# Kernel optimization log

Measured on AMD Instinct MI355X. Metric: run time of the kernel, lower is better.

## Reference

```python
import jax, jax.numpy as jnp
import numpy as np

N = 50000   # nodes
E = 409600  # edges
H = 2       # heads
C = 64      # per-head channels


def _seg_softmax(alpha, dst, n):
    # PyG-style softmax over edges grouped by destination node. alpha: [E, H]
    m = jax.ops.segment_max(alpha, dst, num_segments=n)
    m = jnp.where(jnp.isfinite(m), m, 0.0)
    ex = jnp.exp(alpha - m[dst])
    s = jax.ops.segment_sum(ex, dst, num_segments=n)
    return ex / (s[dst] + 1e-16)


def _tconv(x, src, dst, e, Wq, bq, Wk, bk, Wv, bv, We, Ws, bs, n):
    # PyG TransformerConv (concat=True, beta=False, root_weight=True, dropout=0)
    q = (x @ Wq + bq).reshape(n, H, C)
    k = (x @ Wk + bk).reshape(n, H, C)
    v = (x @ Wv + bv).reshape(n, H, C)
    eh = (e @ We).reshape(-1, H, C)          # lin_edge has no bias in PyG
    kj = k[src] + eh                          # [E, H, C]
    alpha = (q[dst] * kj).sum(-1) / jnp.sqrt(jnp.float32(C))  # [E, H]
    alpha = _seg_softmax(alpha, dst, n)
    msg = (v[src] + eh) * alpha[:, :, None]   # [E, H, C]
    out = jax.ops.segment_sum(msg, dst, num_segments=n).reshape(n, H * C)
    return out + x @ Ws + bs                  # root/skip connection


def setup_inputs() -> dict:
    key = jax.random.key(0)
    ks = jax.random.split(key, 32)

    def lin_w(k, i, o):
        return (jax.random.normal(k, (i, o), dtype=jnp.float32) / np.sqrt(i)).astype(jnp.float32)

    inp = {
        "x": jax.random.normal(ks[0], (N, 6), dtype=jnp.float32),
        "edge_index": jax.random.randint(ks[1], (2, E), 0, N, dtype=jnp.int32).astype(jnp.int64),
        "edge_attr": jax.random.normal(ks[2], (E, 1), dtype=jnp.float32),
        # edge encoder: Linear(1, 64)
        "We_enc": lin_w(ks[3], 1, 64), "be_enc": jnp.zeros((64,), jnp.float32),
        # conv1: TransformerConv(6, 64, heads=2, edge_dim=64)
        "Wq1": lin_w(ks[4], 6, H * C), "bq1": jnp.zeros((H * C,), jnp.float32),
        "Wk1": lin_w(ks[5], 6, H * C), "bk1": jnp.zeros((H * C,), jnp.float32),
        "Wv1": lin_w(ks[6], 6, H * C), "bv1": jnp.zeros((H * C,), jnp.float32),
        "We1": lin_w(ks[7], 64, H * C),
        "Ws1": lin_w(ks[8], 6, H * C), "bs1": jnp.zeros((H * C,), jnp.float32),
        # conv2: TransformerConv(128, 64, heads=2, edge_dim=64)
        "Wq2": lin_w(ks[9], 128, H * C), "bq2": jnp.zeros((H * C,), jnp.float32),
        "Wk2": lin_w(ks[10], 128, H * C), "bk2": jnp.zeros((H * C,), jnp.float32),
        "Wv2": lin_w(ks[11], 128, H * C), "bv2": jnp.zeros((H * C,), jnp.float32),
        "We2": lin_w(ks[12], 64, H * C),
        "Ws2": lin_w(ks[13], 128, H * C), "bs2": jnp.zeros((H * C,), jnp.float32),
        # fc: Linear(128, 1)
        "Wfc": lin_w(ks[14], 128, 1), "bfc": jnp.zeros((1,), jnp.float32),
    }
    return inp


def reference(x, edge_index, edge_attr,
              We_enc, be_enc,
              Wq1, bq1, Wk1, bk1, Wv1, bv1, We1, Ws1, bs1,
              Wq2, bq2, Wk2, bk2, Wv2, bv2, We2, Ws2, bs2,
              Wfc, bfc):
    src, dst = edge_index[0], edge_index[1]
    e = edge_attr @ We_enc + be_enc           # [E, 64]
    h = jax.nn.relu(_tconv(x, src, dst, e, Wq1, bq1, Wk1, bk1, Wv1, bv1, We1, Ws1, bs1, N))
    h = jax.nn.relu(_tconv(h, src, dst, e, Wq2, bq2, Wk2, bk2, Wv2, bv2, We2, Ws2, bs2, N))
    return h @ Wfc + bfc                      # [N, 1]
```

## Files before the change

kernel.cpp:

```cpp
#include <hip/hip_runtime.h>


#define HC 128

typedef __attribute__((ext_vector_type(8))) short bf16x8;
typedef __attribute__((ext_vector_type(4))) float f32x4;
#if __has_builtin(__builtin_amdgcn_fdot2_f32_bf16)
typedef __attribute__((ext_vector_type(2))) __bf16 bf16x2;
#define HAS_DOT2 1
#else
#define HAS_DOT2 0
#endif

__device__ __forceinline__ unsigned bf16_rne(float f) {
    unsigned u = __float_as_uint(f);
    return (u + 0x7fffu + ((u >> 16) & 1u)) >> 16;
}
__device__ __forceinline__ float blo(unsigned u) { return __uint_as_float(u << 16); }
__device__ __forceinline__ float bhi(unsigned u) { return __uint_as_float(u & 0xffff0000u); }

__global__ void k_uc(const float* __restrict__ We_enc, const float* __restrict__ be_enc,
                     const float* __restrict__ We1, const float* __restrict__ We2,
                     float* __restrict__ uc) {
    int c = threadIdx.x;
    float u1 = 0.f, c1 = 0.f, u2 = 0.f, c2 = 0.f;
    for (int j = 0; j < 64; ++j) {
        float we = We_enc[j], be = be_enc[j];
        float w1 = We1[j * HC + c], w2 = We2[j * HC + c];
        u1 += we * w1; c1 += be * w1;
        u2 += we * w2; c2 += be * w2;
    }
    uc[c] = u1; uc[HC + c] = c1; uc[2 * HC + c] = u2; uc[3 * HC + c] = c2;
}

__global__ __launch_bounds__(256) void k_wpack(
    const float* __restrict__ Wq, const float* __restrict__ Wk,
    const float* __restrict__ Wv, const float* __restrict__ Ws,
    unsigned short* __restrict__ Bph) {
    int t = blockIdx.x * 256 + threadIdx.x;
    int nn = t >> 7;
    int kk = t & 127;
    int mat = nn >> 7, c = nn & 127;
    const float* W = (mat == 0) ? Wq : (mat == 1) ? Wk : (mat == 2) ? Wv : Ws;
    Bph[nn * 128 + kk] = (unsigned short)bf16_rne(W[kk * 128 + c]);
}

__global__ __launch_bounds__(256) void k_hist(const int* __restrict__ ei, int* __restrict__ deg, int E) {
    int t = blockIdx.x * blockDim.x + threadIdx.x;
    if (t < E) atomicAdd(&deg[ei[E + t]], 1);
}

__global__ __launch_bounds__(256) void k_scan1(const int* __restrict__ deg, int* __restrict__ bsum, int n) {
    int t = blockIdx.x * 256 + threadIdx.x;
    int v = (t < n) ? deg[t] : 0;
#pragma unroll
    for (int off = 1; off < 64; off <<= 1) v += __shfl_xor(v, off);
    __shared__ int wsum[4];
    int lane = threadIdx.x & 63, w = threadIdx.x >> 6;
    if (lane == 0) wsum[w] = v;
    __syncthreads();
    if (threadIdx.x == 0) bsum[blockIdx.x] = wsum[0] + wsum[1] + wsum[2] + wsum[3];
}

__global__ __launch_bounds__(256) void k_scan2(int* __restrict__ bsum, int nb) {
    __shared__ int sh[256];
    int t = threadIdx.x;
    int v = (t < nb) ? bsum[t] : 0;
    sh[t] = v;
    __syncthreads();
    for (int off = 1; off < 256; off <<= 1) {
        int x = (t >= off) ? sh[t - off] : 0;
        __syncthreads();
        sh[t] += x;
        __syncthreads();
    }
    if (t < nb) bsum[t] = sh[t] - v;
}

__global__ __launch_bounds__(256) void k_scan3(int* __restrict__ deg, const int* __restrict__ bsum,
                                               int* __restrict__ rowptr, int n, int E) {
    int t = blockIdx.x * 256 + threadIdx.x;
    int tid = threadIdx.x;
    int v = (t < n) ? deg[t] : 0;
    __shared__ int sh[256];
    sh[tid] = v;
    __syncthreads();
    for (int off = 1; off < 256; off <<= 1) {
        int x = (tid >= off) ? sh[tid - off] : 0;
        __syncthreads();
        sh[tid] += x;
        __syncthreads();
    }
    if (t < n) { rowptr[t] = bsum[blockIdx.x] + sh[tid] - v; deg[t] = 0; }
    if (t == 0) rowptr[n] = E;
}

__global__ __launch_bounds__(256) void k_scatter(
    const int* __restrict__ ei, const float* __restrict__ ea,
    const int* __restrict__ rowptr, int* __restrict__ cursor,
    int* __restrict__ srcs, float* __restrict__ eas, int E) {
    int t = blockIdx.x * blockDim.x + threadIdx.x;
    if (t >= E) return;
    int dst = ei[E + t];
    int pos = rowptr[dst] + atomicAdd(&cursor[dst], 1);
    srcs[pos] = ei[t];
    eas[pos] = ea[t];
}

__global__ __launch_bounds__(256) void k_lin6(
    const float* __restrict__ X, int n,
    const float* __restrict__ Wq, const float* __restrict__ bq,
    const float* __restrict__ Wk, const float* __restrict__ bk,
    const float* __restrict__ Wv, const float* __restrict__ bv,
    const float* __restrict__ Ws, const float* __restrict__ bs,
    unsigned short* __restrict__ q16, unsigned short* __restrict__ kv,
    unsigned short* __restrict__ sk) {
    __shared__ float xs[16][6];
    const int base = blockIdx.x * 16;
    const int tid = threadIdx.x;
    for (int i = tid; i < 16 * 6; i += 256) {
        int ni = base + i / 6;
        xs[i / 6][i % 6] = (ni < n) ? X[(size_t)ni * 6 + (i % 6)] : 0.f;
    }
    __syncthreads();
    const int c = tid & 127;
    const int m = tid >> 7;
    const float* WA = m ? Wv : Wq;
    const float* WB = m ? Ws : Wk;
    float accA[16], accB[16];
#pragma unroll
    for (int i = 0; i < 16; ++i) { accA[i] = 0.f; accB[i] = 0.f; }
    for (int j = 0; j < 6; ++j) {
        float w0 = WA[j * HC + c];
        float w1 = WB[j * HC + c];
#pragma unroll
        for (int i = 0; i < 16; ++i) {
            float xv = xs[i][j];
            accA[i] += xv * w0;
            accB[i] += xv * w1;
        }
    }
    if (m == 0) {
        const float bA = bq[c], bB = bk[c];
#pragma unroll
        for (int i = 0; i < 16; ++i) {
            int ni = base + i;
            if (ni < n) {
                q16[(size_t)ni * HC + c] = (unsigned short)bf16_rne(accA[i] + bA);
                kv[(size_t)ni * 256 + c] = (unsigned short)bf16_rne(accB[i] + bB);
            }
        }
    } else {
        const float bA = bv[c], bB = bs[c];
#pragma unroll
        for (int i = 0; i < 16; ++i) {
            int ni = base + i;
            if (ni < n) {
                kv[(size_t)ni * 256 + 128 + c] = (unsigned short)bf16_rne(accA[i] + bA);
                sk[(size_t)ni * HC + c] = (unsigned short)bf16_rne(accB[i] + bB);
            }
        }
    }
}

__global__ __launch_bounds__(256, 4) void k_lin2(
    const unsigned short* __restrict__ hb, const unsigned short* __restrict__ Bph,
    const float* __restrict__ bq, const float* __restrict__ bk,
    const float* __restrict__ bv, const float* __restrict__ bs,
    unsigned short* __restrict__ q16, unsigned short* __restrict__ kv,
    unsigned short* __restrict__ sk, int n) {
    __shared__ unsigned short Bs[128][128];
    const int tid = threadIdx.x;
    const int wid = tid >> 6, l = tid & 63;
    const int la = l & 15, lk = l >> 4;
    const int mb = blockIdx.x * 64;
    int nodeA = mb + wid * 16 + la;
    if (nodeA >= n) nodeA = n - 1;
    const int sw = (la & 7) << 3;
    const int crow0 = mb + wid * 16 + lk * 4;

    bf16x8 areg[4];
#pragma unroll
    for (int ks = 0; ks < 4; ++ks)
        areg[ks] = *(const bf16x8*)&hb[(size_t)nodeA * 128 + lk * 8 + ks * 32];

    for (int cq = 0; cq < 4; ++cq) {
        if (cq) __syncthreads();
        for (int i = tid; i < 128 * 16; i += 256) {
            int kk8 = i & 15;
            int nnl = i >> 4;
            bf16x8 val = *(const bf16x8*)&Bph[((size_t)(cq * 128 + nnl)) * 128 + kk8 * 8];
            int swk = (kk8 ^ (nnl & 7)) * 8;
            *(bf16x8*)&Bs[nnl][swk] = val;
        }
        __syncthreads();

        f32x4 acc[8];
#pragma unroll
        for (int nt = 0; nt < 8; ++nt) acc[nt] = (f32x4){0.f, 0.f, 0.f, 0.f};
#pragma unroll
        for (int ks = 0; ks < 4; ++ks) {
            const int rk = (lk * 8 + ks * 32) ^ sw;
#pragma unroll
            for (int nt = 0; nt < 8; ++nt) {
                bf16x8 Bh = *(const bf16x8*)&Bs[nt * 16 + la][rk];
                acc[nt] = __builtin_amdgcn_mfma_f32_16x16x32_bf16(areg[ks], Bh, acc[nt], 0, 0, 0);
            }
        }
        const float* bias = (cq == 0) ? bq : (cq == 1) ? bk : (cq == 2) ? bv : bs;
#pragma unroll
        for (int nt = 0; nt < 8; ++nt) {
            const int col = nt * 16 + la;
            const float bb = bias[col];
            if (cq == 0 || cq == 3) {
                unsigned short* out = (cq == 0) ? q16 : sk;
#pragma unroll
                for (int j = 0; j < 4; ++j) {
                    int n0 = crow0 + j;
                    if (n0 < n) out[(size_t)n0 * 128 + col] = (unsigned short)bf16_rne(acc[nt][j] + bb);
                }
            } else {
                const int co = (cq == 1) ? col : 128 + col;
#pragma unroll
                for (int j = 0; j < 4; ++j) {
                    int n0 = crow0 + j;
                    if (n0 < n) kv[(size_t)n0 * 256 + co] = (unsigned short)bf16_rne(acc[nt][j] + bb);
                }
            }
        }
    }
}

template <int MODE>
__global__ __launch_bounds__(256) void k_attn(
    const unsigned short* __restrict__ q16, const unsigned short* __restrict__ kvp,
    const int* __restrict__ rowptr, const int* __restrict__ srcs, const float* __restrict__ eas,
    const float* __restrict__ ucu, const float* __restrict__ ucc,
    const unsigned short* __restrict__ io, unsigned short* __restrict__ hb,
    const float* __restrict__ Wfc, const float* __restrict__ bfc,
    float* __restrict__ out, int n) {
    int wid = (int)((blockIdx.x * (size_t)blockDim.x + threadIdx.x) >> 6);
    int lane = threadIdx.x & 63;
    if (wid >= n) return;
    const int grp = lane >> 4;
    const int hl = lane & 15;
    const int ch = hl * 8;

    uint4 qp = *(const uint4*)&q16[(size_t)wid * 128 + ch];
    float qu, qc;
    {
        float qf0 = blo(qp.x), qf1 = bhi(qp.x), qf2 = blo(qp.y), qf3 = bhi(qp.y);
        float qf4 = blo(qp.z), qf5 = bhi(qp.z), qf6 = blo(qp.w), qf7 = bhi(qp.w);
        float4 uA = *(const float4*)&ucu[ch], uB = *(const float4*)&ucu[ch + 4];
        float4 cA = *(const float4*)&ucc[ch], cB = *(const float4*)&ucc[ch + 4];
        qu = qf0 * uA.x + qf1 * uA.y + qf2 * uA.z + qf3 * uA.w
           + qf4 * uB.x + qf5 * uB.y + qf6 * uB.z + qf7 * uB.w;
        qc = qf0 * cA.x + qf1 * cA.y + qf2 * cA.z + qf3 * cA.w
           + qf4 * cB.x + qf5 * cB.y + qf6 * cB.z + qf7 * cB.w;
#pragma unroll
        for (int off = 1; off < 8; off <<= 1) {
            qu += __shfl_xor(qu, off);
            qc += __shfl_xor(qc, off);
        }
    }

    int b = rowptr[wid], e = rowptr[wid + 1];
    float s = 0.f, sea = 0.f;
    float av0 = 0.f, av1 = 0.f, av2 = 0.f, av3 = 0.f;
    float av4 = 0.f, av5 = 0.f, av6 = 0.f, av7 = 0.f;

    if (b < e) {
        int p0 = b + grp;          bool v0 = p0 < e; int c0 = v0 ? p0 : e - 1;
        int p1 = b + 4 + grp;      bool v1 = p1 < e; int c1 = v1 ? p1 : e - 1;
        int s0 = srcs[c0], s1 = srcs[c1];
        float ea0 = eas[c0], ea1 = eas[c1];
        const unsigned short* r0p = &kvp[(size_t)s0 * 256 + ch];
        const unsigned short* r1p = &kvp[(size_t)s1 * 256 + ch];
        uint4 ku0 = *(const uint4*)r0p, vu0 = *(const uint4*)(r0p + 128);
        uint4 ku1 = *(const uint4*)r1p, vu1 = *(const uint4*)(r1p + 128);
        for (int p = b; p < e; p += 4) {
            int p2 = p + 8 + grp;
            bool v2 = p2 < e; int c2 = v2 ? p2 : e - 1;
            int s2 = srcs[c2];
            float ea2 = eas[c2];
            const unsigned short* r2p = &kvp[(size_t)s2 * 256 + ch];
            uint4 ku2 = *(const uint4*)r2p, vu2 = *(const uint4*)(r2p + 128);

            float d;
#if HAS_DOT2
            d = __builtin_amdgcn_fdot2_f32_bf16(
                    __builtin_bit_cast(bf16x2, ku0.x), __builtin_bit_cast(bf16x2, qp.x),
                __builtin_amdgcn_fdot2_f32_bf16(
                    __builtin_bit_cast(bf16x2, ku0.y), __builtin_bit_cast(bf16x2, qp.y),
                __builtin_amdgcn_fdot2_f32_bf16(
                    __builtin_bit_cast(bf16x2, ku0.z), __builtin_bit_cast(bf16x2, qp.z),
                __builtin_amdgcn_fdot2_f32_bf16(
                    __builtin_bit_cast(bf16x2, ku0.w), __builtin_bit_cast(bf16x2, qp.w),
                    0.f, false), false), false), false);
#else
            d = blo(qp.x) * blo(ku0.x) + bhi(qp.x) * bhi(ku0.x)
              + blo(qp.y) * blo(ku0.y) + bhi(qp.y) * bhi(ku0.y)
              + blo(qp.z) * blo(ku0.z) + bhi(qp.z) * bhi(ku0.z)
              + blo(qp.w) * blo(ku0.w) + bhi(qp.w) * bhi(ku0.w);
#endif
            d += __shfl_xor(d, 1); d += __shfl_xor(d, 2); d += __shfl_xor(d, 4);
            float a = v0 ? fminf((d + fmaf(ea0, qu, qc)) * 0.125f, 80.f) : -INFINITY;
            float pw = __expf(a);
            s += pw;
            sea = fmaf(pw, ea0, sea);
            av0 = fmaf(pw, blo(vu0.x), av0);
            av1 = fmaf(pw, bhi(vu0.x), av1);
            av2 = fmaf(pw, blo(vu0.y), av2);
            av3 = fmaf(pw, bhi(vu0.y), av3);
            av4 = fmaf(pw, blo(vu0.z), av4);
            av5 = fmaf(pw, bhi(vu0.z), av5);
            av6 = fmaf(pw, blo(vu0.w), av6);
            av7 = fmaf(pw, bhi(vu0.w), av7);
            ku0 = ku1; vu0 = vu1; ea0 = ea1; v0 = v1;
            ku1 = ku2; vu1 = vu2; ea1 = ea2; v1 = v2;
        }
    }

#pragma unroll
    for (int M = 16; M <= 32; M <<= 1) {
        s += __shfl_xor(s, M);
        sea += __shfl_xor(sea, M);
        av0 += __shfl_xor(av0, M); av1 += __shfl_xor(av1, M);
        av2 += __shfl_xor(av2, M); av3 += __shfl_xor(av3, M);
        av4 += __shfl_xor(av4, M); av5 += __shfl_xor(av5, M);
        av6 += __shfl_xor(av6, M); av7 += __shfl_xor(av7, M);
    }

    float4 uuA = *(const float4*)&ucu[ch], uuB = *(const float4*)&ucu[ch + 4];
    float4 ccA = *(const float4*)&ucc[ch], ccB = *(const float4*)&ucc[ch + 4];
    float inv = 1.f / (s + 1e-16f);
    uint4 skp = *(const uint4*)&io[(size_t)wid * 128 + ch];
    float r0 = fmaxf((av0 + uuA.x * sea + ccA.x * s) * inv + blo(skp.x), 0.f);
    float r1 = fmaxf((av1 + uuA.y * sea + ccA.y * s) * inv + bhi(skp.x), 0.f);
    float r2 = fmaxf((av2 + uuA.z * sea + ccA.z * s) * inv + blo(skp.y), 0.f);
    float r3 = fmaxf((av3 + uuA.w * sea + ccA.w * s) * inv + bhi(skp.y), 0.f);
    float r4 = fmaxf((av4 + uuB.x * sea + ccB.x * s) * inv + blo(skp.z), 0.f);
    float r5 = fmaxf((av5 + uuB.y * sea + ccB.y * s) * inv + bhi(skp.z), 0.f);
    float r6 = fmaxf((av6 + uuB.z * sea + ccB.z * s) * inv + blo(skp.w), 0.f);
    float r7 = fmaxf((av7 + uuB.w * sea + ccB.w * s) * inv + bhi(skp.w), 0.f);

    if (MODE == 1) {
        if (grp == 0) {
            uint4 hv;
            hv.x = bf16_rne(r0) | (bf16_rne(r1) << 16);
            hv.y = bf16_rne(r2) | (bf16_rne(r3) << 16);
            hv.z = bf16_rne(r4) | (bf16_rne(r5) << 16);
            hv.w = bf16_rne(r6) | (bf16_rne(r7) << 16);
            *(uint4*)&hb[(size_t)wid * 128 + ch] = hv;
        }
    } else {
        float4 wfA = *(const float4*)&Wfc[ch];
        float4 wfB = *(const float4*)&Wfc[ch + 4];
        float rr = r0 * wfA.x + r1 * wfA.y + r2 * wfA.z + r3 * wfA.w
                 + r4 * wfB.x + r5 * wfB.y + r6 * wfB.z + r7 * wfB.w;
#pragma unroll
        for (int off = 1; off < 16; off <<= 1) rr += __shfl_xor(rr, off);
        if (lane == 0) out[wid] = rr + bfc[0];
    }
}

extern "C" void kernel_launch(void* const* d_in, const int* in_sizes, int n_in,
                              void* d_out, int out_size, void* d_ws, size_t ws_size,
                              hipStream_t stream) {
    const float* x      = (const float*)d_in[0];
    const int*   ei     = (const int*)d_in[1];
    const float* ea     = (const float*)d_in[2];
    const float* We_enc = (const float*)d_in[3];
    const float* be_enc = (const float*)d_in[4];
    const float* Wq1 = (const float*)d_in[5],  *bq1 = (const float*)d_in[6];
    const float* Wk1 = (const float*)d_in[7],  *bk1 = (const float*)d_in[8];
    const float* Wv1 = (const float*)d_in[9],  *bv1 = (const float*)d_in[10];
    const float* We1 = (const float*)d_in[11];
    const float* Ws1 = (const float*)d_in[12], *bs1 = (const float*)d_in[13];
    const float* Wq2 = (const float*)d_in[14], *bq2 = (const float*)d_in[15];
    const float* Wk2 = (const float*)d_in[16], *bk2 = (const float*)d_in[17];
    const float* Wv2 = (const float*)d_in[18], *bv2 = (const float*)d_in[19];
    const float* We2 = (const float*)d_in[20];
    const float* Ws2 = (const float*)d_in[21], *bs2 = (const float*)d_in[22];
    const float* Wfc = (const float*)d_in[23], *bfc = (const float*)d_in[24];

    const int n = in_sizes[0] / 6;
    const int E = in_sizes[2];

    float* ws = (float*)d_ws;
    size_t off = 0;
    unsigned short* qb16 = (unsigned short*)(ws + off); off += (size_t)n * HC / 2;
    unsigned short* sk16 = (unsigned short*)(ws + off); off += (size_t)n * HC / 2;
    unsigned short* kv16 = (unsigned short*)(ws + off); off += (size_t)n * HC;
    int* rowptr = (int*)(ws + off); off += (size_t)(n + 1);
    int* deg    = (int*)(ws + off); off += (size_t)n;
    int* bsum   = (int*)(ws + off); off += 256;
    int* srcs   = (int*)(ws + off); off += (size_t)E;
    float* eas  = ws + off; off += (size_t)E;
    float* uc   = ws + off; off += 512;
    unsigned short* hb16 = (unsigned short*)(ws + off); off += (size_t)n * HC / 2;
    unsigned short* Bph = (unsigned short*)(ws + off); off += 512 * 128 / 2;

    const int eb = (E + 255) / 256;
    const int nb = (n + 255) / 256;
    const int wb = (int)(((size_t)n * 64 + 255) / 256);

    hipLaunchKernelGGL(k_uc, dim3(1), dim3(128), 0, stream, We_enc, be_enc, We1, We2, uc);
    hipLaunchKernelGGL(k_wpack, dim3(256), dim3(256), 0, stream, Wq2, Wk2, Wv2, Ws2, Bph);

    hipMemsetAsync(deg, 0, (size_t)n * sizeof(int), stream);
    hipLaunchKernelGGL(k_hist, dim3(eb), dim3(256), 0, stream, ei, deg, E);
    hipLaunchKernelGGL(k_scan1, dim3(nb), dim3(256), 0, stream, deg, bsum, n);
    hipLaunchKernelGGL(k_scan2, dim3(1), dim3(256), 0, stream, bsum, nb);
    hipLaunchKernelGGL(k_scan3, dim3(nb), dim3(256), 0, stream, deg, bsum, rowptr, n, E);
    hipLaunchKernelGGL(k_scatter, dim3(eb), dim3(256), 0, stream, ei, ea, rowptr, deg, srcs, eas, E);

    hipLaunchKernelGGL(k_lin6, dim3((n + 15) / 16), dim3(256), 0, stream,
                       x, n, Wq1, bq1, Wk1, bk1, Wv1, bv1, Ws1, bs1, qb16, kv16, sk16);
    hipLaunchKernelGGL((k_attn<1>), dim3(wb), dim3(256), 0, stream,
                       qb16, kv16, rowptr, srcs, eas, uc, uc + HC, sk16, hb16,
                       Wfc, bfc, (float*)d_out, n);

    hipLaunchKernelGGL(k_lin2, dim3((n + 63) / 64), dim3(256), 0, stream,
                       hb16, Bph, bq2, bk2, bv2, bs2, qb16, kv16, sk16, n);
    hipLaunchKernelGGL((k_attn<0>), dim3(wb), dim3(256), 0, stream,
                       qb16, kv16, rowptr, srcs, eas, uc + 2 * HC, uc + 3 * HC, sk16,
                       (unsigned short*)nullptr, Wfc, bfc, (float*)d_out, n);
}
```

Measured before the change: 196.2 us.

## Pack edge src and attr into int2, pad CSR, merge prep kernels

Combines the CSR source index and edge attribute into one int2 array so each edge needs a single 8-byte load. The array gets 16 zeroed padding entries, which lets the attention loop drop the index clamping. The two setup kernels are merged into one launch. Attention kernels now run one 64-thread block per node instead of four wavefronts per 256-thread block. Smaller blocks raise block-scheduling overhead, and out-of-range edges now read padding that points at node 0, so they must still be masked by the validity flags.

```diff
diff --git a/kernel.cpp b/kernel.cpp
--- a/kernel.cpp
+++ b/kernel.cpp
@@ -19,24 +19,26 @@
 __device__ __forceinline__ float blo(unsigned u) { return __uint_as_float(u << 16); }
 __device__ __forceinline__ float bhi(unsigned u) { return __uint_as_float(u & 0xffff0000u); }
 
-__global__ void k_uc(const float* __restrict__ We_enc, const float* __restrict__ be_enc,
-                     const float* __restrict__ We1, const float* __restrict__ We2,
-                     float* __restrict__ uc) {
-    int c = threadIdx.x;
-    float u1 = 0.f, c1 = 0.f, u2 = 0.f, c2 = 0.f;
-    for (int j = 0; j < 64; ++j) {
-        float we = We_enc[j], be = be_enc[j];
-        float w1 = We1[j * HC + c], w2 = We2[j * HC + c];
-        u1 += we * w1; c1 += be * w1;
-        u2 += we * w2; c2 += be * w2;
-    }
-    uc[c] = u1; uc[HC + c] = c1; uc[2 * HC + c] = u2; uc[3 * HC + c] = c2;
-}
-
-__global__ __launch_bounds__(256) void k_wpack(
+__global__ __launch_bounds__(256) void k_prep(
+    const float* __restrict__ We_enc, const float* __restrict__ be_enc,
+    const float* __restrict__ We1, const float* __restrict__ We2,
     const float* __restrict__ Wq, const float* __restrict__ Wk,
     const float* __restrict__ Wv, const float* __restrict__ Ws,
-    unsigned short* __restrict__ Bph) {
+    float* __restrict__ uc, unsigned short* __restrict__ Bph) {
+    if (blockIdx.x == 256) {
+        int c = threadIdx.x;
+        if (c < 128) {
+            float u1 = 0.f, c1 = 0.f, u2 = 0.f, c2 = 0.f;
+            for (int j = 0; j < 64; ++j) {
+                float we = We_enc[j], be = be_enc[j];
+                float w1 = We1[j * HC + c], w2 = We2[j * HC + c];
+                u1 += we * w1; c1 += be * w1;
+                u2 += we * w2; c2 += be * w2;
+            }
+            uc[c] = u1; uc[HC + c] = c1; uc[2 * HC + c] = u2; uc[3 * HC + c] = c2;
+        }
+        return;
+    }
     int t = blockIdx.x * 256 + threadIdx.x;
     int nn = t >> 7;
     int kk = t & 127;
@@ -98,13 +100,13 @@
 __global__ __launch_bounds__(256) void k_scatter(
     const int* __restrict__ ei, const float* __restrict__ ea,
     const int* __restrict__ rowptr, int* __restrict__ cursor,
-    int* __restrict__ srcs, float* __restrict__ eas, int E) {
+    int2* __restrict__ sep, int E) {
     int t = blockIdx.x * blockDim.x + threadIdx.x;
+    if (t < 16 && blockIdx.x == 0) sep[E + t] = make_int2(0, 0);
     if (t >= E) return;
     int dst = ei[E + t];
     int pos = rowptr[dst] + atomicAdd(&cursor[dst], 1);
-    srcs[pos] = ei[t];
-    eas[pos] = ea[t];
+    sep[pos] = make_int2(ei[t], __float_as_int(ea[t]));
 }
 
 __global__ __launch_bounds__(256) void k_lin6(
@@ -232,14 +234,14 @@
 }
 
 template <int MODE>
-__global__ __launch_bounds__(256) void k_attn(
+__global__ __launch_bounds__(64) void k_attn(
     const unsigned short* __restrict__ q16, const unsigned short* __restrict__ kvp,
-    const int* __restrict__ rowptr, const int* __restrict__ srcs, const float* __restrict__ eas,
+    const int* __restrict__ rowptr, const int2* __restrict__ sep,
     const float* __restrict__ ucu, const float* __restrict__ ucc,
     const unsigned short* __restrict__ io, unsigned short* __restrict__ hb,
     const float* __restrict__ Wfc, const float* __restrict__ bfc,
     float* __restrict__ out, int n) {
-    int wid = (int)((blockIdx.x * (size_t)blockDim.x + threadIdx.x) >> 6);
+    int wid = blockIdx.x;
     int lane = threadIdx.x & 63;
     if (wid >= n) return;
     const int grp = lane >> 4;
@@ -270,22 +272,22 @@
     float av4 = 0.f, av5 = 0.f, av6 = 0.f, av7 = 0.f;
 
     if (b < e) {
-        int p0 = b + grp;          bool v0 = p0 < e; int c0 = v0 ? p0 : e - 1;
-        int p1 = b + 4 + grp;      bool v1 = p1 < e; int c1 = v1 ? p1 : e - 1;
-        int s0 = srcs[c0], s1 = srcs[c1];
-        float ea0 = eas[c0], ea1 = eas[c1];
-        const unsigned short* r0p = &kvp[(size_t)s0 * 256 + ch];
-        const unsigned short* r1p = &kvp[(size_t)s1 * 256 + ch];
+        int p0 = b + grp;      bool v0 = p0 < e;
+        int p1 = p0 + 4;       bool v1 = p1 < e;
+        int2 se0 = sep[p0];
+        int2 se1 = sep[p1];
+        const unsigned short* r0p = &kvp[(size_t)se0.x * 256 + ch];
+        const unsigned short* r1p = &kvp[(size_t)se1.x * 256 + ch];
         uint4 ku0 = *(const uint4*)r0p, vu0 = *(const uint4*)(r0p + 128);
         uint4 ku1 = *(const uint4*)r1p, vu1 = *(const uint4*)(r1p + 128);
         for (int p = b; p < e; p += 4) {
             int p2 = p + 8 + grp;
-            bool v2 = p2 < e; int c2 = v2 ? p2 : e - 1;
-            int s2 = srcs[c2];
-            float ea2 = eas[c2];
-            const unsigned short* r2p = &kvp[(size_t)s2 * 256 + ch];
+            bool v2 = p2 < e;
+            int2 se2 = sep[p2];
+            const unsigned short* r2p = &kvp[(size_t)se2.x * 256 + ch];
             uint4 ku2 = *(const uint4*)r2p, vu2 = *(const uint4*)(r2p + 128);
 
+            float ea0 = __int_as_float(se0.y);
             float d;
 #if HAS_DOT2
             d = __builtin_amdgcn_fdot2_f32_bf16(
@@ -316,8 +318,8 @@
             av5 = fmaf(pw, bhi(vu0.z), av5);
             av6 = fmaf(pw, blo(vu0.w), av6);
             av7 = fmaf(pw, bhi(vu0.w), av7);
-            ku0 = ku1; vu0 = vu1; ea0 = ea1; v0 = v1;
-            ku1 = ku2; vu1 = vu2; ea1 = ea2; v1 = v2;
+            ku0 = ku1; vu0 = vu1; se0 = se1; v0 = v1;
+            ku1 = ku2; vu1 = vu2; se1 = se2; v1 = v2;
         }
     }
 
@@ -395,35 +397,33 @@
     int* rowptr = (int*)(ws + off); off += (size_t)(n + 1);
     int* deg    = (int*)(ws + off); off += (size_t)n;
     int* bsum   = (int*)(ws + off); off += 256;
-    int* srcs   = (int*)(ws + off); off += (size_t)E;
-    float* eas  = ws + off; off += (size_t)E;
+    int2* sep   = (int2*)(ws + off); off += 2 * ((size_t)E + 16);
     float* uc   = ws + off; off += 512;
     unsigned short* hb16 = (unsigned short*)(ws + off); off += (size_t)n * HC / 2;
     unsigned short* Bph = (unsigned short*)(ws + off); off += 512 * 128 / 2;
 
     const int eb = (E + 255) / 256;
     const int nb = (n + 255) / 256;
-    const int wb = (int)(((size_t)n * 64 + 255) / 256);
-
-    hipLaunchKernelGGL(k_uc, dim3(1), dim3(128), 0, stream, We_enc, be_enc, We1, We2, uc);
-    hipLaunchKernelGGL(k_wpack, dim3(256), dim3(256), 0, stream, Wq2, Wk2, Wv2, Ws2, Bph);
+
+    hipLaunchKernelGGL(k_prep, dim3(257), dim3(256), 0, stream,
+                       We_enc, be_enc, We1, We2, Wq2, Wk2, Wv2, Ws2, uc, Bph);
 
     hipMemsetAsync(deg, 0, (size_t)n * sizeof(int), stream);
     hipLaunchKernelGGL(k_hist, dim3(eb), dim3(256), 0, stream, ei, deg, E);
     hipLaunchKernelGGL(k_scan1, dim3(nb), dim3(256), 0, stream, deg, bsum, n);
     hipLaunchKernelGGL(k_scan2, dim3(1), dim3(256), 0, stream, bsum, nb);
     hipLaunchKernelGGL(k_scan3, dim3(nb), dim3(256), 0, stream, deg, bsum, rowptr, n, E);
-    hipLaunchKernelGGL(k_scatter, dim3(eb), dim3(256), 0, stream, ei, ea, rowptr, deg, srcs, eas, E);
+    hipLaunchKernelGGL(k_scatter, dim3(eb), dim3(256), 0, stream, ei, ea, rowptr, deg, sep, E);
 
     hipLaunchKernelGGL(k_lin6, dim3((n + 15) / 16), dim3(256), 0, stream,
                        x, n, Wq1, bq1, Wk1, bk1, Wv1, bv1, Ws1, bs1, qb16, kv16, sk16);
-    hipLaunchKernelGGL((k_attn<1>), dim3(wb), dim3(256), 0, stream,
-                       qb16, kv16, rowptr, srcs, eas, uc, uc + HC, sk16, hb16,
+    hipLaunchKernelGGL((k_attn<1>), dim3(n), dim3(64), 0, stream,
+                       qb16, kv16, rowptr, sep, uc, uc + HC, sk16, hb16,
                        Wfc, bfc, (float*)d_out, n);
 
     hipLaunchKernelGGL(k_lin2, dim3((n + 63) / 64), dim3(256), 0, stream,
                        hb16, Bph, bq2, bk2, bv2, bs2, qb16, kv16, sk16, n);
-    hipLaunchKernelGGL((k_attn<0>), dim3(wb), dim3(256), 0, stream,
-                       qb16, kv16, rowptr, srcs, eas, uc + 2 * HC, uc + 3 * HC, sk16,
+    hipLaunchKernelGGL((k_attn<0>), dim3(n), dim3(64), 0, stream,
+                       qb16, kv16, rowptr, sep, uc + 2 * HC, uc + 3 * HC, sk16,
                        (unsigned short*)nullptr, Wfc, bfc, (float*)d_out, n);
 }
```

Result: faster. 190.6 us, median of 2 (-2.9%).
